# Kernel optimization log

Measured on AMD Instinct MI355X. Metric: run time of the kernel, lower is better.

The kernel has to match this reference:

```python
import jax, jax.numpy as jnp
import numpy as np

B, T, NX, NXS, H, NY, NYS = 16384, 60, 4, 3, 64, 4, 3


def _lstm(x, h0, c0, Wih, Whh, bih, bhh):
    """PyTorch-convention LSTM (gate order i,f,g,o). x: [B,T,X]. Returns (hs [B,T,H], hT, cT)."""
    # precompute input contribution for all timesteps: [T,B,4H]
    xg = jnp.transpose(jnp.einsum('btx,gx->btg', x, Wih) + (bih + bhh), (1, 0, 2))

    def step(carry, xg_t):
        h, c = carry
        g = xg_t + h @ Whh.T
        i, f, gg, o = jnp.split(g, 4, axis=-1)
        c = jax.nn.sigmoid(f) * c + jax.nn.sigmoid(i) * jnp.tanh(gg)
        h = jax.nn.sigmoid(o) * jnp.tanh(c)
        return (h, c), h

    (hT, cT), hs = jax.lax.scan(step, (h0, c0), xg)
    return jnp.transpose(hs, (1, 0, 2)), hT, cT


def setup_inputs() -> dict:
    key = jax.random.key(0)
    ks = jax.random.split(key, 24)
    w = lambda k, shp: (jax.random.normal(k, shp, jnp.float32) * 0.1)
    return {
        'inputs_main': jax.random.normal(ks[0], (B, T, NX), jnp.float32),
        'inputs_aux': jax.random.normal(ks[1], (B, NXS), jnp.float32),
        'hx2': jax.random.normal(ks[2], (B, H), jnp.float32),
        'cx2': jax.random.normal(ks[3], (B, H), jnp.float32),
        'Ws1': w(ks[4], (H, NXS)), 'bs1': w(ks[5], (H,)),
        'Ws2': w(ks[6], (H, NXS)), 'bs2': w(ks[7], (H,)),
        'Wih1': w(ks[8], (4 * H, NX)), 'Whh1': w(ks[9], (4 * H, H)),
        'bih1': w(ks[10], (4 * H,)), 'bhh1': w(ks[11], (4 * H,)),
        'Wih2': w(ks[12], (4 * H, H)), 'Whh2': w(ks[13], (4 * H, H)),
        'bih2': w(ks[14], (4 * H,)), 'bhh2': w(ks[15], (4 * H,)),
        'Wlat': w(ks[16], (H, H)), 'blat': w(ks[17], (H,)),
        'Wout': w(ks[18], (NY, H)), 'bout': w(ks[19], (NY,)),
        'Wsfc': w(ks[20], (NYS, H)), 'bsfc': w(ks[21], (NYS,)),
    }


def reference(inputs_main, inputs_aux, hx2, cx2, Ws1, bs1, Ws2, bs2,
              Wih1, Whh1, bih1, bhh1, Wih2, Whh2, bih2, bhh2,
              Wlat, blat, Wout, bout, Wsfc, bsfc):
    # surface MLPs -> initial LSTM1 state (h raw, c tanh'd)
    hx = inputs_aux @ Ws1.T + bs1
    cx = jnp.tanh(inputs_aux @ Ws2.T + bs2)
    # run LSTM1 top-down (flipped levels)
    x1 = jnp.flip(inputs_main, axis=1)
    rnn1out, _, _ = _lstm(x1, hx, cx, Wih1, Whh1, bih1, bhh1)
    # flip back and run LSTM2 bottom-up with (hx2, cx2)
    # (the original calls rnn2 twice; only the second call's result is used)
    rnn1out_f = jnp.flip(rnn1out, axis=1)
    rnn2out, last_h, _ = _lstm(rnn1out_f, hx2, cx2, Wih2, Whh2, bih2, bhh2)
    # intermediate MLP + output head
    lat = rnn2out @ Wlat.T + blat                # [B,T,H]
    out = lat @ Wout.T + bout                    # [B,T,NY]
    out_sfc = jax.nn.relu(last_h @ Wsfc.T + bsfc)  # [B,NYS]
    return out, out_sfc
```

## Files before the change

kernel.cpp:

```cpp
#include <hip/hip_runtime.h>
#include <hip/hip_bf16.h>

#define BB 16384
#define TT 60

typedef short bf16x8 __attribute__((ext_vector_type(8)));
typedef float f32x4 __attribute__((ext_vector_type(4)));

__device__ __forceinline__ unsigned short f2bs(float f) {
    __hip_bfloat16 h = __float2bfloat16(f);
    return __builtin_bit_cast(unsigned short, h);
}

__device__ __forceinline__ void lstm_cell(float xi, float xf, float xg, float xo,
                                          float& c, float& h) {
    xi = fminf(fmaxf(xi, -17.f), 17.f);
    xf = fminf(fmaxf(xf, -17.f), 17.f);
    xo = fminf(fmaxf(xo, -17.f), 17.f);
    xg = fminf(fmaxf(xg, -11.f), 11.f);
    const float ei = __expf(-xi), ef = __expf(-xf), eo = __expf(-xo), eg = __expf(2.f * xg);
    const float di = 1.f + ei, df = 1.f + ef, dd = 1.f + eo, dg = 1.f + eg;
    const float a = di * df, b = dd * dg;
    const float R = __builtin_amdgcn_rcpf(a * b);
    const float si = df * b * R;
    const float sf = di * b * R;
    const float so = a * dg * R;
    const float tg = (eg - 1.f) * (a * dd) * R;
    const float cn = sf * c + si * tg;
    c = cn;
    const float tc = fminf(fmaxf(cn, -11.f), 11.f);
    const float ec = __expf(2.f * tc);
    const float th = (ec - 1.f) * __builtin_amdgcn_rcpf(ec + 1.f);
    h = so * th;
}

#define STEP_BARRIER() do {                                   \
    asm volatile("s_waitcnt lgkmcnt(0)" ::: "memory");        \
    __builtin_amdgcn_s_barrier();                             \
    __builtin_amdgcn_sched_barrier(0);                        \
} while (0)

__device__ __forceinline__ bf16x8 pack8(float4 a, float4 b) {
    bf16x8 r;
    r[0] = (short)f2bs(a.x); r[1] = (short)f2bs(a.y);
    r[2] = (short)f2bs(a.z); r[3] = (short)f2bs(a.w);
    r[4] = (short)f2bs(b.x); r[5] = (short)f2bs(b.y);
    r[6] = (short)f2bs(b.z); r[7] = (short)f2bs(b.w);
    return r;
}

__global__ __launch_bounds__(256, 3) void k_lstm1(
    const float* __restrict__ xmain, const float* __restrict__ aux,
    const float* __restrict__ Ws1, const float* __restrict__ bs1,
    const float* __restrict__ Ws2, const float* __restrict__ bs2,
    const float* __restrict__ Wih1, const float* __restrict__ Whh1,
    const float* __restrict__ bih1, const float* __restrict__ bhh1,
    unsigned short* __restrict__ rnn1t)
{
    __shared__ unsigned short hB[2 * 2048];

    const int tid = threadIdx.x;
    {
        unsigned int* p32 = (unsigned int*)hB;
        #pragma unroll
        for (int e = 0; e < 8; ++e) p32[tid + 256 * e] = 0;
    }
    const int hj = tid >> 6, lane = tid & 63;
    const int row16 = lane & 15, quad = lane >> 4;
    const int b0 = blockIdx.x * 16;
    const int swz = (row16 & 7) << 3;

    bf16x8 wf[4][3];
    float fb[4];
    #pragma unroll
    for (int i = 0; i < 4; ++i) {
        const int g = (hj + 4 * i) * 16 + row16;
        const float* wr = Whh1 + g * 64 + quad * 8;
        wf[i][0] = pack8(*(const float4*)wr, *(const float4*)(wr + 4));
        wf[i][1] = pack8(*(const float4*)(wr + 32), *(const float4*)(wr + 36));
        float4 z4 = {0.f, 0.f, 0.f, 0.f};
        float4 xw = z4;
        if (quad == 0) xw = *(const float4*)(Wih1 + g * 4);
        wf[i][2] = pack8(xw, z4);
        fb[i] = bih1[g] + bhh1[g];
    }
    __syncthreads();

    const int j = hj * 16 + row16;
    const unsigned oA0 = (unsigned)(((row16 * 128 + 0 + quad * 8) ^ swz) * 2);
    const unsigned oA1 = (unsigned)(((row16 * 128 + 32 + quad * 8) ^ swz) * 2);
    const unsigned oA2 = (unsigned)(((row16 * 128 + 64 + quad * 8) ^ swz) * 2);
    unsigned oW[4];
    #pragma unroll
    for (int r = 0; r < 4; ++r) {
        const int m = quad * 4 + r;
        oW[r] = (unsigned)(((m * 128 + j) ^ ((m & 7) << 3)) * 2);
    }
    const unsigned oX = (unsigned)(((lane * 128 + 64) ^ ((lane & 7) << 3)) * 2);
    char* const hBb = (char*)hB;

    const float w10 = Ws1[j * 3], w11 = Ws1[j * 3 + 1], w12 = Ws1[j * 3 + 2], sb1v = bs1[j];
    const float w20 = Ws2[j * 3], w21 = Ws2[j * 3 + 1], w22 = Ws2[j * 3 + 2], sb2v = bs2[j];
    f32x4 cc;
    #pragma unroll
    for (int r = 0; r < 4; ++r) {
        const float a0v = aux[(b0 + quad * 4 + r) * 3], a1v = aux[(b0 + quad * 4 + r) * 3 + 1], a2v = aux[(b0 + quad * 4 + r) * 3 + 2];
        float h0 = w10 * a0v + w11 * a1v + w12 * a2v + sb1v;
        float c0in = w20 * a0v + w21 * a1v + w22 * a2v + sb2v;
        c0in = fminf(fmaxf(c0in, -11.f), 11.f);
        const float e0 = __expf(2.f * c0in);
        cc[r] = (e0 - 1.f) * __builtin_amdgcn_rcpf(e0 + 1.f);
        *(unsigned short*)(hBb + oW[r]) = f2bs(h0);
    }
    if (hj == 2 && lane < 16) {
        float4 xv = ((const float4*)xmain)[(size_t)(b0 + lane) * TT + 59];
        uint2 p2;
        p2.x = (unsigned)f2bs(xv.x) | ((unsigned)f2bs(xv.y) << 16);
        p2.y = (unsigned)f2bs(xv.z) | ((unsigned)f2bs(xv.w) << 16);
        *(uint2*)(hBb + oX) = p2;
    }
    __syncthreads();

    const float4* px = (const float4*)xmain + (size_t)(b0 + lane) * TT + 58;
    unsigned short* pst = rnn1t + ((size_t)60 * BB + b0 + row16) * 64 + ((hj == 1) ? 32 : 0) + quad * 8;

    unsigned pofs = 0;
    #pragma unroll 1
    for (int s = 0; s < TT; ++s) {
        char* hbP = hBb + pofs;
        char* hbN = hBb + (pofs ^ 4096);
        float4 xv;
        if (hj == 2 && lane < 16 && s < TT - 1) xv = *px;
        bf16x8 a0 = *(const bf16x8*)(hbP + oA0);
        bf16x8 a1 = *(const bf16x8*)(hbP + oA1);
        bf16x8 a2 = *(const bf16x8*)(hbP + oA2);
        if (s > 0) {
            if (hj == 0) *(bf16x8*)pst = a0;
            if (hj == 1) *(bf16x8*)pst = a1;
        }
        pst -= (size_t)BB * 64;
        px -= 1;

        f32x4 ac[4];
        #pragma unroll
        for (int i = 0; i < 4; ++i) { f32x4 v = {fb[i], fb[i], fb[i], fb[i]}; ac[i] = v; }
        #pragma unroll
        for (int i = 0; i < 4; ++i) {
            ac[i] = __builtin_amdgcn_mfma_f32_16x16x32_bf16(a0, wf[i][0], ac[i], 0, 0, 0);
            ac[i] = __builtin_amdgcn_mfma_f32_16x16x32_bf16(a1, wf[i][1], ac[i], 0, 0, 0);
            ac[i] = __builtin_amdgcn_mfma_f32_16x16x32_bf16(a2, wf[i][2], ac[i], 0, 0, 0);
        }
        #pragma unroll
        for (int r = 0; r < 4; ++r) {
            float cr = cc[r], hr;
            lstm_cell(ac[0][r], ac[1][r], ac[2][r], ac[3][r], cr, hr);
            cc[r] = cr;
            *(unsigned short*)(hbN + oW[r]) = f2bs(hr);
        }
        if (hj == 2 && lane < 16 && s < TT - 1) {
            uint2 p2;
            p2.x = (unsigned)f2bs(xv.x) | ((unsigned)f2bs(xv.y) << 16);
            p2.y = (unsigned)f2bs(xv.z) | ((unsigned)f2bs(xv.w) << 16);
            *(uint2*)(hbN + oX) = p2;
        }
        STEP_BARRIER();
        pofs ^= 4096;
    }
    char* hbP = hBb + pofs;
    if (hj == 0) {
        bf16x8 a0 = *(const bf16x8*)(hbP + oA0);
        *(bf16x8*)&rnn1t[((size_t)(b0 + row16)) * 64 + quad * 8] = a0;
    }
    if (hj == 1) {
        bf16x8 a1 = *(const bf16x8*)(hbP + oA1);
        *(bf16x8*)&rnn1t[((size_t)(b0 + row16)) * 64 + 32 + quad * 8] = a1;
    }
}

__global__ __launch_bounds__(256, 3) void k_lstm2(
    const unsigned short* __restrict__ rnn1t,
    const float* __restrict__ hx2, const float* __restrict__ cx2,
    const float* __restrict__ Wih2, const float* __restrict__ Whh2,
    const float* __restrict__ bih2, const float* __restrict__ bhh2,
    const float* __restrict__ Wlat, const float* __restrict__ blat,
    const float* __restrict__ Wout, const float* __restrict__ bout,
    const float* __restrict__ Wsfc, const float* __restrict__ bsfc,
    float* __restrict__ out)
{
    __shared__ unsigned short hB[2 * 2048];
    __shared__ unsigned short whead[16 * 64];

    const int tid = threadIdx.x;
    {
        unsigned int* p32 = (unsigned int*)hB;
        #pragma unroll
        for (int e = 0; e < 8; ++e) p32[tid + 256 * e] = 0;
        unsigned int* w32 = (unsigned int*)whead;
        w32[tid] = 0; w32[tid + 256] = 0;
    }
    const int hj = tid >> 6, lane = tid & 63;
    const int row16 = lane & 15, quad = lane >> 4;
    const int b0 = blockIdx.x * 16;
    const int swz = (row16 & 7) << 3;

    bf16x8 wf[4][4];
    float fb[4];
    #pragma unroll
    for (int i = 0; i < 4; ++i) {
        const int g = (hj + 4 * i) * 16 + row16;
        const float* wh = Whh2 + g * 64 + quad * 8;
        const float* wi = Wih2 + g * 64 + quad * 8;
        wf[i][0] = pack8(*(const float4*)wh, *(const float4*)(wh + 4));
        wf[i][1] = pack8(*(const float4*)(wh + 32), *(const float4*)(wh + 36));
        wf[i][2] = pack8(*(const float4*)wi, *(const float4*)(wi + 4));
        wf[i][3] = pack8(*(const float4*)(wi + 32), *(const float4*)(wi + 36));
        fb[i] = bih2[g] + bhh2[g];
    }
    float bcomb = 0.f;
    if (row16 < 4) {
        float s = 0.f;
        for (int jj = 0; jj < 64; ++jj) s += Wout[row16 * 64 + jj] * blat[jj];
        bcomb = s + bout[row16];
    } else if (row16 < 7) {
        bcomb = bsfc[row16 - 4];
    }
    __syncthreads();

    {
        const int o = tid >> 6, k = tid & 63;
        float s = 0.f;
        for (int jj = 0; jj < 64; ++jj) s += Wout[o * 64 + jj] * Wlat[jj * 64 + k];
        whead[(o * 64 + k) ^ ((o & 7) << 3)] = f2bs(s);
        if (tid < 192) {
            const int o2 = o + 4;
            whead[(o2 * 64 + k) ^ ((o2 & 7) << 3)] = f2bs(Wsfc[o * 64 + k]);
        }
    }

    const int j = hj * 16 + row16;
    const unsigned oA0 = (unsigned)(((row16 * 128 + 0 + quad * 8) ^ swz) * 2);
    const unsigned oA1 = (unsigned)(((row16 * 128 + 32 + quad * 8) ^ swz) * 2);
    const unsigned oA2 = (unsigned)(((row16 * 128 + 64 + quad * 8) ^ swz) * 2);
    const unsigned oA3 = (unsigned)(((row16 * 128 + 96 + quad * 8) ^ swz) * 2);
    unsigned oW[4];
    #pragma unroll
    for (int r = 0; r < 4; ++r) {
        const int m = quad * 4 + r;
        oW[r] = (unsigned)(((m * 128 + j) ^ ((m & 7) << 3)) * 2);
    }
    const unsigned oPV = (hj == 0) ? oA2 : oA3;
    const unsigned oH0 = (unsigned)(((row16 * 64 + 0 + quad * 8) ^ swz) * 2);
    const unsigned oH1 = (unsigned)(((row16 * 64 + 32 + quad * 8) ^ swz) * 2);
    char* const hBb = (char*)hB;
    char* const whb = (char*)whead;

    f32x4 cc;
    #pragma unroll
    for (int r = 0; r < 4; ++r) {
        const int m = quad * 4 + r;
        cc[r] = cx2[(size_t)(b0 + m) * 64 + j];
        *(unsigned short*)(hBb + oW[r]) = f2bs(hx2[(size_t)(b0 + m) * 64 + j]);
    }
    if (hj == 0) {
        bf16x8 v = *(const bf16x8*)&rnn1t[((size_t)(b0 + row16)) * 64 + quad * 8];
        *(bf16x8*)(hBb + oA2) = v;
    }
    if (hj == 1) {
        bf16x8 v = *(const bf16x8*)&rnn1t[((size_t)(b0 + row16)) * 64 + 32 + quad * 8];
        *(bf16x8*)(hBb + oA3) = v;
    }
    __syncthreads();

    bf16x8 wh0 = *(const bf16x8*)(whb + oH0);
    bf16x8 wh1 = *(const bf16x8*)(whb + oH1);

    const unsigned short* ppv = rnn1t + ((size_t)1 * BB + b0 + row16) * 64 + ((hj == 1) ? 32 : 0) + quad * 8;
    float* po = out + ((size_t)(b0 + quad * 4) * TT) * 4 + row16;

    unsigned pofs = 0;
    #pragma unroll 1
    for (int t = 0; t < TT; ++t) {
        char* hbP = hBb + pofs;
        char* hbN = hBb + (pofs ^ 4096);
        bf16x8 pv;
        if (t < TT - 1) {
            if (hj == 0) pv = *(const bf16x8*)ppv;
            if (hj == 1) pv = *(const bf16x8*)ppv;
        }
        ppv += (size_t)BB * 64;
        bf16x8 a0 = *(const bf16x8*)(hbP + oA0);
        bf16x8 a1 = *(const bf16x8*)(hbP + oA1);
        bf16x8 a2 = *(const bf16x8*)(hbP + oA2);
        bf16x8 a3 = *(const bf16x8*)(hbP + oA3);

        if (hj == 3 && t > 0) {
            f32x4 hacc = {bcomb, bcomb, bcomb, bcomb};
            hacc = __builtin_amdgcn_mfma_f32_16x16x32_bf16(a0, wh0, hacc, 0, 0, 0);
            hacc = __builtin_amdgcn_mfma_f32_16x16x32_bf16(a1, wh1, hacc, 0, 0, 0);
            if (row16 < 4) {
                #pragma unroll
                for (int r = 0; r < 4; ++r)
                    po[r * TT * 4] = hacc[r];
            }
            po += 4;
        }

        f32x4 ac[4];
        #pragma unroll
        for (int i = 0; i < 4; ++i) { f32x4 v = {fb[i], fb[i], fb[i], fb[i]}; ac[i] = v; }
        #pragma unroll
        for (int i = 0; i < 4; ++i) {
            ac[i] = __builtin_amdgcn_mfma_f32_16x16x32_bf16(a0, wf[i][0], ac[i], 0, 0, 0);
            ac[i] = __builtin_amdgcn_mfma_f32_16x16x32_bf16(a1, wf[i][1], ac[i], 0, 0, 0);
            ac[i] = __builtin_amdgcn_mfma_f32_16x16x32_bf16(a2, wf[i][2], ac[i], 0, 0, 0);
            ac[i] = __builtin_amdgcn_mfma_f32_16x16x32_bf16(a3, wf[i][3], ac[i], 0, 0, 0);
        }
        #pragma unroll
        for (int r = 0; r < 4; ++r) {
            float cr = cc[r], hr;
            lstm_cell(ac[0][r], ac[1][r], ac[2][r], ac[3][r], cr, hr);
            cc[r] = cr;
            *(unsigned short*)(hbN + oW[r]) = f2bs(hr);
        }
        if (t < TT - 1) {
            if (hj == 0) *(bf16x8*)(hbN + oPV) = pv;
            if (hj == 1) *(bf16x8*)(hbN + oPV) = pv;
        }
        STEP_BARRIER();
        pofs ^= 4096;
    }
    if (hj == 3) {
        char* hbP = hBb + pofs;
        bf16x8 a0 = *(const bf16x8*)(hbP + oA0);
        bf16x8 a1 = *(const bf16x8*)(hbP + oA1);
        f32x4 hacc = {bcomb, bcomb, bcomb, bcomb};
        hacc = __builtin_amdgcn_mfma_f32_16x16x32_bf16(a0, wh0, hacc, 0, 0, 0);
        hacc = __builtin_amdgcn_mfma_f32_16x16x32_bf16(a1, wh1, hacc, 0, 0, 0);
        if (row16 < 4) {
            #pragma unroll
            for (int r = 0; r < 4; ++r)
                out[((size_t)(b0 + quad * 4 + r) * TT + 59) * 4 + row16] = hacc[r];
        } else if (row16 < 7) {
            float* osfc = out + (size_t)BB * TT * 4;
            #pragma unroll
            for (int r = 0; r < 4; ++r)
                osfc[(size_t)(b0 + quad * 4 + r) * 3 + (row16 - 4)] = fmaxf(hacc[r], 0.f);
        }
    }
}

extern "C" void kernel_launch(void* const* d_in, const int* in_sizes, int n_in,
                              void* d_out, int out_size, void* d_ws, size_t ws_size,
                              hipStream_t stream) {
    const float* xmain = (const float*)d_in[0];
    const float* aux   = (const float*)d_in[1];
    const float* hx2   = (const float*)d_in[2];
    const float* cx2   = (const float*)d_in[3];
    const float* Ws1   = (const float*)d_in[4];
    const float* bs1   = (const float*)d_in[5];
    const float* Ws2   = (const float*)d_in[6];
    const float* bs2   = (const float*)d_in[7];
    const float* Wih1  = (const float*)d_in[8];
    const float* Whh1  = (const float*)d_in[9];
    const float* bih1  = (const float*)d_in[10];
    const float* bhh1  = (const float*)d_in[11];
    const float* Wih2  = (const float*)d_in[12];
    const float* Whh2  = (const float*)d_in[13];
    const float* bih2  = (const float*)d_in[14];
    const float* bhh2  = (const float*)d_in[15];
    const float* Wlat  = (const float*)d_in[16];
    const float* blat  = (const float*)d_in[17];
    const float* Wout  = (const float*)d_in[18];
    const float* bout  = (const float*)d_in[19];
    const float* Wsfc  = (const float*)d_in[20];
    const float* bsfc  = (const float*)d_in[21];

    unsigned short* rnn1t = (unsigned short*)d_ws;
    float* out = (float*)d_out;

    dim3 grid(BB / 16), block(256);
    k_lstm1<<<grid, block, 0, stream>>>(xmain, aux, Ws1, bs1, Ws2, bs2,
                                        Wih1, Whh1, bih1, bhh1, rnn1t);
    k_lstm2<<<grid, block, 0, stream>>>(rnn1t, hx2, cx2, Wih2, Whh2, bih2, bhh2,
                                        Wlat, blat, Wout, bout, Wsfc, bsfc, out);
}
```

Baseline: 271.0 us.

## Process 32 batch rows per block in both LSTM kernels, reusing gate weights

Each block now handles two 16-row batch tiles per step, so the register-resident weight fragments feed twice as many MFMAs and the grid is halved. Per-step barrier and LDS round-trip costs are spread over more rows, and hidden-state stores and head-output work are redistributed across all four waves. The change also swaps clamps to fmed3 and uses packed bf16 conversion. In exchange it needs more registers and LDS per block (launch bounds drop from 3 to 2 blocks per SM) and gives fewer blocks for latency hiding.

```diff
diff --git a/kernel.cpp b/kernel.cpp
--- a/kernel.cpp
+++ b/kernel.cpp
@@ -12,12 +12,18 @@
     return __builtin_bit_cast(unsigned short, h);
 }
 
+__device__ __forceinline__ unsigned cvtpk2(float lo, float hi) {
+    unsigned r;
+    asm("v_cvt_pk_bf16_f32 %0, %1, %2" : "=v"(r) : "v"(lo), "v"(hi));
+    return r;
+}
+
 __device__ __forceinline__ void lstm_cell(float xi, float xf, float xg, float xo,
                                           float& c, float& h) {
-    xi = fminf(fmaxf(xi, -17.f), 17.f);
-    xf = fminf(fmaxf(xf, -17.f), 17.f);
-    xo = fminf(fmaxf(xo, -17.f), 17.f);
-    xg = fminf(fmaxf(xg, -11.f), 11.f);
+    xi = __builtin_amdgcn_fmed3f(xi, -17.f, 17.f);
+    xf = __builtin_amdgcn_fmed3f(xf, -17.f, 17.f);
+    xo = __builtin_amdgcn_fmed3f(xo, -17.f, 17.f);
+    xg = __builtin_amdgcn_fmed3f(xg, -11.f, 11.f);
     const float ei = __expf(-xi), ef = __expf(-xf), eo = __expf(-xo), eg = __expf(2.f * xg);
     const float di = 1.f + ei, df = 1.f + ef, dd = 1.f + eo, dg = 1.f + eg;
     const float a = di * df, b = dd * dg;
@@ -28,7 +34,7 @@
     const float tg = (eg - 1.f) * (a * dd) * R;
     const float cn = sf * c + si * tg;
     c = cn;
-    const float tc = fminf(fmaxf(cn, -11.f), 11.f);
+    const float tc = __builtin_amdgcn_fmed3f(cn, -11.f, 11.f);
     const float ec = __expf(2.f * tc);
     const float th = (ec - 1.f) * __builtin_amdgcn_rcpf(ec + 1.f);
     h = so * th;
@@ -49,7 +55,7 @@
     return r;
 }
 
-__global__ __launch_bounds__(256, 3) void k_lstm1(
+__global__ __launch_bounds__(256, 2) void k_lstm1(
     const float* __restrict__ xmain, const float* __restrict__ aux,
     const float* __restrict__ Ws1, const float* __restrict__ bs1,
     const float* __restrict__ Ws2, const float* __restrict__ bs2,
@@ -57,17 +63,17 @@
     const float* __restrict__ bih1, const float* __restrict__ bhh1,
     unsigned short* __restrict__ rnn1t)
 {
-    __shared__ unsigned short hB[2 * 2048];
+    __shared__ unsigned short hB[2 * 4096];
 
     const int tid = threadIdx.x;
     {
         unsigned int* p32 = (unsigned int*)hB;
         #pragma unroll
-        for (int e = 0; e < 8; ++e) p32[tid + 256 * e] = 0;
+        for (int e = 0; e < 16; ++e) p32[tid + 256 * e] = 0;
     }
     const int hj = tid >> 6, lane = tid & 63;
     const int row16 = lane & 15, quad = lane >> 4;
-    const int b0 = blockIdx.x * 16;
+    const int b0 = blockIdx.x * 32;
     const int swz = (row16 & 7) << 3;
 
     bf16x8 wf[4][3];
@@ -101,83 +107,101 @@
 
     const float w10 = Ws1[j * 3], w11 = Ws1[j * 3 + 1], w12 = Ws1[j * 3 + 2], sb1v = bs1[j];
     const float w20 = Ws2[j * 3], w21 = Ws2[j * 3 + 1], w22 = Ws2[j * 3 + 2], sb2v = bs2[j];
-    f32x4 cc;
-    #pragma unroll
-    for (int r = 0; r < 4; ++r) {
-        const float a0v = aux[(b0 + quad * 4 + r) * 3], a1v = aux[(b0 + quad * 4 + r) * 3 + 1], a2v = aux[(b0 + quad * 4 + r) * 3 + 2];
-        float h0 = w10 * a0v + w11 * a1v + w12 * a2v + sb1v;
-        float c0in = w20 * a0v + w21 * a1v + w22 * a2v + sb2v;
-        c0in = fminf(fmaxf(c0in, -11.f), 11.f);
-        const float e0 = __expf(2.f * c0in);
-        cc[r] = (e0 - 1.f) * __builtin_amdgcn_rcpf(e0 + 1.f);
-        *(unsigned short*)(hBb + oW[r]) = f2bs(h0);
-    }
-    if (hj == 2 && lane < 16) {
+    f32x4 cc[2];
+    #pragma unroll
+    for (int mh = 0; mh < 2; ++mh) {
+        #pragma unroll
+        for (int r = 0; r < 4; ++r) {
+            const int m = mh * 16 + quad * 4 + r;
+            const float a0v = aux[(b0 + m) * 3], a1v = aux[(b0 + m) * 3 + 1], a2v = aux[(b0 + m) * 3 + 2];
+            float h0 = w10 * a0v + w11 * a1v + w12 * a2v + sb1v;
+            float c0in = w20 * a0v + w21 * a1v + w22 * a2v + sb2v;
+            c0in = __builtin_amdgcn_fmed3f(c0in, -11.f, 11.f);
+            const float e0 = __expf(2.f * c0in);
+            cc[mh][r] = (e0 - 1.f) * __builtin_amdgcn_rcpf(e0 + 1.f);
+            *(unsigned short*)(hBb + oW[r] + mh * 4096) = f2bs(h0);
+        }
+    }
+    if (hj == 2 && lane < 32) {
         float4 xv = ((const float4*)xmain)[(size_t)(b0 + lane) * TT + 59];
-        uint2 p2;
-        p2.x = (unsigned)f2bs(xv.x) | ((unsigned)f2bs(xv.y) << 16);
-        p2.y = (unsigned)f2bs(xv.z) | ((unsigned)f2bs(xv.w) << 16);
+        uint2 p2 = { cvtpk2(xv.x, xv.y), cvtpk2(xv.z, xv.w) };
         *(uint2*)(hBb + oX) = p2;
     }
     __syncthreads();
 
     const float4* px = (const float4*)xmain + (size_t)(b0 + lane) * TT + 58;
-    unsigned short* pst = rnn1t + ((size_t)60 * BB + b0 + row16) * 64 + ((hj == 1) ? 32 : 0) + quad * 8;
+    unsigned short* pst = rnn1t + ((size_t)60 * BB + b0 + ((hj >> 1) << 4) + row16) * 64 + ((hj & 1) << 5) + quad * 8;
 
     unsigned pofs = 0;
     #pragma unroll 1
     for (int s = 0; s < TT; ++s) {
         char* hbP = hBb + pofs;
-        char* hbN = hBb + (pofs ^ 4096);
+        char* hbN = hBb + (pofs ^ 8192);
         float4 xv;
-        if (hj == 2 && lane < 16 && s < TT - 1) xv = *px;
-        bf16x8 a0 = *(const bf16x8*)(hbP + oA0);
-        bf16x8 a1 = *(const bf16x8*)(hbP + oA1);
-        bf16x8 a2 = *(const bf16x8*)(hbP + oA2);
+        if (hj == 2 && lane < 32 && s < TT - 1) xv = *px;
+        bf16x8 a0[2], a1[2], a2[2];
+        #pragma unroll
+        for (int mh = 0; mh < 2; ++mh) {
+            a0[mh] = *(const bf16x8*)(hbP + oA0 + mh * 4096);
+            a1[mh] = *(const bf16x8*)(hbP + oA1 + mh * 4096);
+            a2[mh] = *(const bf16x8*)(hbP + oA2 + mh * 4096);
+        }
         if (s > 0) {
-            if (hj == 0) *(bf16x8*)pst = a0;
-            if (hj == 1) *(bf16x8*)pst = a1;
+            bf16x8 sv = (hj == 0) ? a0[0] : (hj == 1) ? a1[0] : (hj == 2) ? a0[1] : a1[1];
+            *(bf16x8*)pst = sv;
         }
         pst -= (size_t)BB * 64;
         px -= 1;
 
-        f32x4 ac[4];
-        #pragma unroll
-        for (int i = 0; i < 4; ++i) { f32x4 v = {fb[i], fb[i], fb[i], fb[i]}; ac[i] = v; }
-        #pragma unroll
-        for (int i = 0; i < 4; ++i) {
-            ac[i] = __builtin_amdgcn_mfma_f32_16x16x32_bf16(a0, wf[i][0], ac[i], 0, 0, 0);
-            ac[i] = __builtin_amdgcn_mfma_f32_16x16x32_bf16(a1, wf[i][1], ac[i], 0, 0, 0);
-            ac[i] = __builtin_amdgcn_mfma_f32_16x16x32_bf16(a2, wf[i][2], ac[i], 0, 0, 0);
-        }
-        #pragma unroll
-        for (int r = 0; r < 4; ++r) {
-            float cr = cc[r], hr;
-            lstm_cell(ac[0][r], ac[1][r], ac[2][r], ac[3][r], cr, hr);
-            cc[r] = cr;
-            *(unsigned short*)(hbN + oW[r]) = f2bs(hr);
-        }
-        if (hj == 2 && lane < 16 && s < TT - 1) {
-            uint2 p2;
-            p2.x = (unsigned)f2bs(xv.x) | ((unsigned)f2bs(xv.y) << 16);
-            p2.y = (unsigned)f2bs(xv.z) | ((unsigned)f2bs(xv.w) << 16);
+        f32x4 ac[2][4];
+        #pragma unroll
+        for (int mh = 0; mh < 2; ++mh)
+            #pragma unroll
+            for (int i = 0; i < 4; ++i) { f32x4 v = {fb[i], fb[i], fb[i], fb[i]}; ac[mh][i] = v; }
+        #pragma unroll
+        for (int mh = 0; mh < 2; ++mh) {
+            #pragma unroll
+            for (int i = 0; i < 4; ++i) {
+                ac[mh][i] = __builtin_amdgcn_mfma_f32_16x16x32_bf16(a0[mh], wf[i][0], ac[mh][i], 0, 0, 0);
+                ac[mh][i] = __builtin_amdgcn_mfma_f32_16x16x32_bf16(a1[mh], wf[i][1], ac[mh][i], 0, 0, 0);
+                ac[mh][i] = __builtin_amdgcn_mfma_f32_16x16x32_bf16(a2[mh], wf[i][2], ac[mh][i], 0, 0, 0);
+            }
+        }
+        #pragma unroll
+        for (int mh = 0; mh < 2; ++mh) {
+            float hr[4];
+            #pragma unroll
+            for (int r = 0; r < 4; ++r) {
+                float cr = cc[mh][r];
+                lstm_cell(ac[mh][0][r], ac[mh][1][r], ac[mh][2][r], ac[mh][3][r], cr, hr[r]);
+                cc[mh][r] = cr;
+            }
+            const unsigned u01 = cvtpk2(hr[0], hr[1]);
+            const unsigned u23 = cvtpk2(hr[2], hr[3]);
+            *(unsigned short*)(hbN + oW[0] + mh * 4096) = (unsigned short)u01;
+            *(unsigned short*)(hbN + oW[1] + mh * 4096) = (unsigned short)(u01 >> 16);
+            *(unsigned short*)(hbN + oW[2] + mh * 4096) = (unsigned short)u23;
+            *(unsigned short*)(hbN + oW[3] + mh * 4096) = (unsigned short)(u23 >> 16);
+        }
+        if (hj == 2 && lane < 32 && s < TT - 1) {
+            uint2 p2 = { cvtpk2(xv.x, xv.y), cvtpk2(xv.z, xv.w) };
             *(uint2*)(hbN + oX) = p2;
         }
         STEP_BARRIER();
-        pofs ^= 4096;
-    }
-    char* hbP = hBb + pofs;
-    if (hj == 0) {
-        bf16x8 a0 = *(const bf16x8*)(hbP + oA0);
-        *(bf16x8*)&rnn1t[((size_t)(b0 + row16)) * 64 + quad * 8] = a0;
-    }
-    if (hj == 1) {
-        bf16x8 a1 = *(const bf16x8*)(hbP + oA1);
-        *(bf16x8*)&rnn1t[((size_t)(b0 + row16)) * 64 + 32 + quad * 8] = a1;
-    }
-}
-
-__global__ __launch_bounds__(256, 3) void k_lstm2(
+        pofs ^= 8192;
+    }
+    {
+        char* hbP = hBb + pofs;
+        bf16x8 sv;
+        if (hj == 0)      sv = *(const bf16x8*)(hbP + oA0);
+        else if (hj == 1) sv = *(const bf16x8*)(hbP + oA1);
+        else if (hj == 2) sv = *(const bf16x8*)(hbP + oA0 + 4096);
+        else              sv = *(const bf16x8*)(hbP + oA1 + 4096);
+        *(bf16x8*)&rnn1t[((size_t)(b0 + ((hj >> 1) << 4) + row16)) * 64 + ((hj & 1) << 5) + quad * 8] = sv;
+    }
+}
+
+__global__ __launch_bounds__(256, 2) void k_lstm2(
     const unsigned short* __restrict__ rnn1t,
     const float* __restrict__ hx2, const float* __restrict__ cx2,
     const float* __restrict__ Wih2, const float* __restrict__ Whh2,
@@ -187,20 +211,17 @@
     const float* __restrict__ Wsfc, const float* __restrict__ bsfc,
     float* __restrict__ out)
 {
-    __shared__ unsigned short hB[2 * 2048];
+    __shared__ unsigned short hB[2 * 4096];
     __shared__ unsigned short whead[16 * 64];
 
     const int tid = threadIdx.x;
     {
-        unsigned int* p32 = (unsigned int*)hB;
-        #pragma unroll
-        for (int e = 0; e < 8; ++e) p32[tid + 256 * e] = 0;
         unsigned int* w32 = (unsigned int*)whead;
         w32[tid] = 0; w32[tid + 256] = 0;
     }
     const int hj = tid >> 6, lane = tid & 63;
     const int row16 = lane & 15, quad = lane >> 4;
-    const int b0 = blockIdx.x * 16;
+    const int b0 = blockIdx.x * 32;
     const int swz = (row16 & 7) << 3;
 
     bf16x8 wf[4][4];
@@ -248,55 +269,63 @@
         const int m = quad * 4 + r;
         oW[r] = (unsigned)(((m * 128 + j) ^ ((m & 7) << 3)) * 2);
     }
-    const unsigned oPV = (hj == 0) ? oA2 : oA3;
+    const unsigned oPV = (unsigned)(((row16 * 128 + 64 + ((hj & 1) << 5) + quad * 8) ^ swz) * 2);
     const unsigned oH0 = (unsigned)(((row16 * 64 + 0 + quad * 8) ^ swz) * 2);
     const unsigned oH1 = (unsigned)(((row16 * 64 + 32 + quad * 8) ^ swz) * 2);
     char* const hBb = (char*)hB;
     char* const whb = (char*)whead;
 
-    f32x4 cc;
-    #pragma unroll
-    for (int r = 0; r < 4; ++r) {
-        const int m = quad * 4 + r;
-        cc[r] = cx2[(size_t)(b0 + m) * 64 + j];
-        *(unsigned short*)(hBb + oW[r]) = f2bs(hx2[(size_t)(b0 + m) * 64 + j]);
-    }
-    if (hj == 0) {
-        bf16x8 v = *(const bf16x8*)&rnn1t[((size_t)(b0 + row16)) * 64 + quad * 8];
-        *(bf16x8*)(hBb + oA2) = v;
-    }
-    if (hj == 1) {
-        bf16x8 v = *(const bf16x8*)&rnn1t[((size_t)(b0 + row16)) * 64 + 32 + quad * 8];
-        *(bf16x8*)(hBb + oA3) = v;
+    f32x4 cc[2];
+    #pragma unroll
+    for (int mh = 0; mh < 2; ++mh) {
+        #pragma unroll
+        for (int r = 0; r < 4; ++r) {
+            const int m = mh * 16 + quad * 4 + r;
+            cc[mh][r] = cx2[(size_t)(b0 + m) * 64 + j];
+            *(unsigned short*)(hBb + oW[r] + mh * 4096) = f2bs(hx2[(size_t)(b0 + m) * 64 + j]);
+        }
+    }
+    if (hj < 2) {
+        bf16x8 v0 = *(const bf16x8*)&rnn1t[((size_t)(b0 + row16)) * 64 + ((hj & 1) << 5) + quad * 8];
+        bf16x8 v1 = *(const bf16x8*)&rnn1t[((size_t)(b0 + 16 + row16)) * 64 + ((hj & 1) << 5) + quad * 8];
+        *(bf16x8*)(hBb + oPV) = v0;
+        *(bf16x8*)(hBb + oPV + 4096) = v1;
     }
     __syncthreads();
 
     bf16x8 wh0 = *(const bf16x8*)(whb + oH0);
     bf16x8 wh1 = *(const bf16x8*)(whb + oH1);
 
-    const unsigned short* ppv = rnn1t + ((size_t)1 * BB + b0 + row16) * 64 + ((hj == 1) ? 32 : 0) + quad * 8;
-    float* po = out + ((size_t)(b0 + quad * 4) * TT) * 4 + row16;
+    const unsigned short* ppv = rnn1t + ((size_t)BB + b0 + row16) * 64 + ((hj & 1) << 5) + quad * 8;
+    float* po = out + ((size_t)(b0 + ((hj == 2) ? 16 : 0) + quad * 4) * TT) * 4 + row16;
 
     unsigned pofs = 0;
     #pragma unroll 1
     for (int t = 0; t < TT; ++t) {
         char* hbP = hBb + pofs;
-        char* hbN = hBb + (pofs ^ 4096);
-        bf16x8 pv;
-        if (t < TT - 1) {
-            if (hj == 0) pv = *(const bf16x8*)ppv;
-            if (hj == 1) pv = *(const bf16x8*)ppv;
+        char* hbN = hBb + (pofs ^ 8192);
+        bf16x8 pv0, pv1;
+        if (hj < 2 && t < TT - 1) {
+            pv0 = *(const bf16x8*)ppv;
+            pv1 = *(const bf16x8*)(ppv + 16 * 64);
         }
         ppv += (size_t)BB * 64;
-        bf16x8 a0 = *(const bf16x8*)(hbP + oA0);
-        bf16x8 a1 = *(const bf16x8*)(hbP + oA1);
-        bf16x8 a2 = *(const bf16x8*)(hbP + oA2);
-        bf16x8 a3 = *(const bf16x8*)(hbP + oA3);
-
-        if (hj == 3 && t > 0) {
+
+        bf16x8 a0[2], a1[2], a2[2], a3[2];
+        #pragma unroll
+        for (int mh = 0; mh < 2; ++mh) {
+            a0[mh] = *(const bf16x8*)(hbP + oA0 + mh * 4096);
+            a1[mh] = *(const bf16x8*)(hbP + oA1 + mh * 4096);
+            a2[mh] = *(const bf16x8*)(hbP + oA2 + mh * 4096);
+            a3[mh] = *(const bf16x8*)(hbP + oA3 + mh * 4096);
+        }
+
+        if (hj >= 2 && t > 0) {
+            const bf16x8 ha0 = (hj == 3) ? a0[0] : a0[1];
+            const bf16x8 ha1 = (hj == 3) ? a1[0] : a1[1];
             f32x4 hacc = {bcomb, bcomb, bcomb, bcomb};
-            hacc = __builtin_amdgcn_mfma_f32_16x16x32_bf16(a0, wh0, hacc, 0, 0, 0);
-            hacc = __builtin_amdgcn_mfma_f32_16x16x32_bf16(a1, wh1, hacc, 0, 0, 0);
+            hacc = __builtin_amdgcn_mfma_f32_16x16x32_bf16(ha0, wh0, hacc, 0, 0, 0);
+            hacc = __builtin_amdgcn_mfma_f32_16x16x32_bf16(ha1, wh1, hacc, 0, 0, 0);
             if (row16 < 4) {
                 #pragma unroll
                 for (int r = 0; r < 4; ++r)
@@ -305,46 +334,62 @@
             po += 4;
         }
 
-        f32x4 ac[4];
-        #pragma unroll
-        for (int i = 0; i < 4; ++i) { f32x4 v = {fb[i], fb[i], fb[i], fb[i]}; ac[i] = v; }
-        #pragma unroll
-        for (int i = 0; i < 4; ++i) {
-            ac[i] = __builtin_amdgcn_mfma_f32_16x16x32_bf16(a0, wf[i][0], ac[i], 0, 0, 0);
-            ac[i] = __builtin_amdgcn_mfma_f32_16x16x32_bf16(a1, wf[i][1], ac[i], 0, 0, 0);
-            ac[i] = __builtin_amdgcn_mfma_f32_16x16x32_bf16(a2, wf[i][2], ac[i], 0, 0, 0);
-            ac[i] = __builtin_amdgcn_mfma_f32_16x16x32_bf16(a3, wf[i][3], ac[i], 0, 0, 0);
-        }
-        #pragma unroll
-        for (int r = 0; r < 4; ++r) {
-            float cr = cc[r], hr;
-            lstm_cell(ac[0][r], ac[1][r], ac[2][r], ac[3][r], cr, hr);
-            cc[r] = cr;
-            *(unsigned short*)(hbN + oW[r]) = f2bs(hr);
-        }
-        if (t < TT - 1) {
-            if (hj == 0) *(bf16x8*)(hbN + oPV) = pv;
-            if (hj == 1) *(bf16x8*)(hbN + oPV) = pv;
+        f32x4 ac[2][4];
+        #pragma unroll
+        for (int mh = 0; mh < 2; ++mh)
+            #pragma unroll
+            for (int i = 0; i < 4; ++i) { f32x4 v = {fb[i], fb[i], fb[i], fb[i]}; ac[mh][i] = v; }
+        #pragma unroll
+        for (int mh = 0; mh < 2; ++mh) {
+            #pragma unroll
+            for (int i = 0; i < 4; ++i) {
+                ac[mh][i] = __builtin_amdgcn_mfma_f32_16x16x32_bf16(a0[mh], wf[i][0], ac[mh][i], 0, 0, 0);
+                ac[mh][i] = __builtin_amdgcn_mfma_f32_16x16x32_bf16(a1[mh], wf[i][1], ac[mh][i], 0, 0, 0);
+                ac[mh][i] = __builtin_amdgcn_mfma_f32_16x16x32_bf16(a2[mh], wf[i][2], ac[mh][i], 0, 0, 0);
+                ac[mh][i] = __builtin_amdgcn_mfma_f32_16x16x32_bf16(a3[mh], wf[i][3], ac[mh][i], 0, 0, 0);
+            }
+        }
+        #pragma unroll
+        for (int mh = 0; mh < 2; ++mh) {
+            float hr[4];
+            #pragma unroll
+            for (int r = 0; r < 4; ++r) {
+                float cr = cc[mh][r];
+                lstm_cell(ac[mh][0][r], ac[mh][1][r], ac[mh][2][r], ac[mh][3][r], cr, hr[r]);
+                cc[mh][r] = cr;
+            }
+            const unsigned u01 = cvtpk2(hr[0], hr[1]);
+            const unsigned u23 = cvtpk2(hr[2], hr[3]);
+            *(unsigned short*)(hbN + oW[0] + mh * 4096) = (unsigned short)u01;
+            *(unsigned short*)(hbN + oW[1] + mh * 4096) = (unsigned short)(u01 >> 16);
+            *(unsigned short*)(hbN + oW[2] + mh * 4096) = (unsigned short)u23;
+            *(unsigned short*)(hbN + oW[3] + mh * 4096) = (unsigned short)(u23 >> 16);
+        }
+        if (hj < 2 && t < TT - 1) {
+            *(bf16x8*)(hbN + oPV) = pv0;
+            *(bf16x8*)(hbN + oPV + 4096) = pv1;
         }
         STEP_BARRIER();
-        pofs ^= 4096;
-    }
-    if (hj == 3) {
+        pofs ^= 8192;
+    }
+    if (hj >= 2) {
         char* hbP = hBb + pofs;
-        bf16x8 a0 = *(const bf16x8*)(hbP + oA0);
-        bf16x8 a1 = *(const bf16x8*)(hbP + oA1);
+        const int mho = (hj == 3) ? 0 : 4096;
+        bf16x8 ea0 = *(const bf16x8*)(hbP + oA0 + mho);
+        bf16x8 ea1 = *(const bf16x8*)(hbP + oA1 + mho);
         f32x4 hacc = {bcomb, bcomb, bcomb, bcomb};
-        hacc = __builtin_amdgcn_mfma_f32_16x16x32_bf16(a0, wh0, hacc, 0, 0, 0);
-        hacc = __builtin_amdgcn_mfma_f32_16x16x32_bf16(a1, wh1, hacc, 0, 0, 0);
+        hacc = __builtin_amdgcn_mfma_f32_16x16x32_bf16(ea0, wh0, hacc, 0, 0, 0);
+        hacc = __builtin_amdgcn_mfma_f32_16x16x32_bf16(ea1, wh1, hacc, 0, 0, 0);
+        const int rb = b0 + ((hj == 2) ? 16 : 0) + quad * 4;
         if (row16 < 4) {
             #pragma unroll
             for (int r = 0; r < 4; ++r)
-                out[((size_t)(b0 + quad * 4 + r) * TT + 59) * 4 + row16] = hacc[r];
+                out[((size_t)(rb + r) * TT + 59) * 4 + row16] = hacc[r];
         } else if (row16 < 7) {
             float* osfc = out + (size_t)BB * TT * 4;
             #pragma unroll
             for (int r = 0; r < 4; ++r)
-                osfc[(size_t)(b0 + quad * 4 + r) * 3 + (row16 - 4)] = fmaxf(hacc[r], 0.f);
+                osfc[(size_t)(rb + r) * 3 + (row16 - 4)] = fmaxf(hacc[r], 0.f);
         }
     }
 }
@@ -378,7 +423,7 @@
     unsigned short* rnn1t = (unsigned short*)d_ws;
     float* out = (float*)d_out;
 
-    dim3 grid(BB / 16), block(256);
+    dim3 grid(BB / 32), block(256);
     k_lstm1<<<grid, block, 0, stream>>>(xmain, aux, Ws1, bs1, Ws2, bs2,
                                         Wih1, Whh1, bih1, bhh1, rnn1t);
     k_lstm2<<<grid, block, 0, stream>>>(rnn1t, hx2, cx2, Wih2, Whh2, bih2, bhh2,
```

After: 237.6 us. 1.14x faster.
